# Kernel tuning notes

Hardware: AMD Instinct MI355X
Metric: run time of the kernel (lower is better)

The kernel has to match this reference:

```python
import jax, jax.numpy as jnp
import numpy as np

INPUT_SIZE = (224, 224)


def setup_inputs() -> dict:
    key = jax.random.key(0)
    k1, k2, k3 = jax.random.split(key, 3)
    feat2 = jax.random.normal(k1, (16, 512, 28, 28), dtype=jnp.float32)
    feat3 = jax.random.normal(k2, (16, 1024, 14, 14), dtype=jnp.float32)
    memory_bank = jax.random.normal(k3, (16384, 1536), dtype=jnp.float32)
    return {"feat2": feat2, "feat3": feat3, "memory_bank": memory_bank}


def reference(feat2, feat3, memory_bank):
    b, c2, h, w = feat2.shape
    c3 = feat3.shape[1]
    # interpolate(feat3, size=(h,w), mode='bilinear', align_corners=False)
    feat3_up = jax.image.resize(feat3, (b, c3, h, w), method='bilinear')
    features = jnp.concatenate([feat2, feat3_up], axis=1)  # [b, c, h, w]
    c = c2 + c3
    feats = features.transpose(0, 2, 3, 1).reshape(-1, c)  # [N, c]
    x_sq = jnp.sum(feats * feats, axis=1, keepdims=True)            # [N, 1]
    m_sq = jnp.sum(memory_bank * memory_bank, axis=1)[None, :]      # [1, M]
    d2 = x_sq + m_sq - 2.0 * (feats @ memory_bank.T)                # [N, M]
    min_d = jnp.sqrt(jnp.maximum(jnp.min(d2, axis=1), 0.0))         # [N]
    anomaly_map = min_d.reshape(b, 1, h, w)
    anomaly_map = jax.image.resize(
        anomaly_map, (b, 1, INPUT_SIZE[0], INPUT_SIZE[1]), method='bilinear')
    pred_score = jnp.max(anomaly_map.reshape(b, -1), axis=1)
    return anomaly_map, pred_score
```

## Files before the change

kernel.cpp:

```cpp
#include <hip/hip_runtime.h>
#include <math.h>

#define N_ROWS 12544
#define C_DIM  1536
#define M_ROWS 16384
#define BATCH  16

#define QS    16.0f
#define S2x2  0.0078125f
#define S2    0.00390625f

typedef int   i32x4 __attribute__((ext_vector_type(4)));
typedef unsigned char u8;
typedef signed char   i8;

__device__ __forceinline__ unsigned fkey(float f) {
  unsigned u = __float_as_uint(f);
  return (u & 0x80000000u) ? ~u : (u | 0x80000000u);
}
__device__ __forceinline__ float funkey(unsigned k) {
  unsigned u = (k & 0x80000000u) ? (k ^ 0x80000000u) : ~k;
  return __uint_as_float(u);
}

__device__ __forceinline__ void gl_lds16(const void* g, void* l) {
  __builtin_amdgcn_global_load_lds(
      (__attribute__((address_space(1))) void*)(g),
      (__attribute__((address_space(3))) void*)(l), 16, 0, 0);
}

__device__ __forceinline__ int quant(float v) {
  int q = __float2int_rn(v * QS);
  return max(-127, min(127, q));
}

__global__ void prep_all(const float* __restrict__ feat2,
                         const float* __restrict__ feat3,
                         const float* __restrict__ mb,
                         i8* __restrict__ feats, i8* __restrict__ mbb,
                         float* __restrict__ xsq, float* __restrict__ msq,
                         unsigned* __restrict__ dmin,
                         unsigned* __restrict__ score) {
  const int blk = blockIdx.x;
  const int t = threadIdx.x;
  __shared__ float sred[4];

  if (blk < M_ROWS) {
    const int j = blk;
    const float* in = mb + (size_t)j * C_DIM;
    i8* outp = mbb + (size_t)j * C_DIM;
    float ssq = 0.f;
    {
      const float4 v = *(const float4*)(in + t * 4);
      int q0 = quant(v.x), q1 = quant(v.y), q2 = quant(v.z), q3 = quant(v.w);
      unsigned w = (unsigned)(q0 & 0xFF) | ((unsigned)(q1 & 0xFF) << 8)
                 | ((unsigned)(q2 & 0xFF) << 16) | ((unsigned)(q3 & 0xFF) << 24);
      *(unsigned*)(outp + t * 4) = w;
      ssq = (float)(q0*q0 + q1*q1 + q2*q2 + q3*q3);
    }
    if (t < 128) {
      const int i2 = 256 + t;
      const float4 v = *(const float4*)(in + i2 * 4);
      int q0 = quant(v.x), q1 = quant(v.y), q2 = quant(v.z), q3 = quant(v.w);
      unsigned w = (unsigned)(q0 & 0xFF) | ((unsigned)(q1 & 0xFF) << 8)
                 | ((unsigned)(q2 & 0xFF) << 16) | ((unsigned)(q3 & 0xFF) << 24);
      *(unsigned*)(outp + i2 * 4) = w;
      ssq += (float)(q0*q0 + q1*q1 + q2*q2 + q3*q3);
    }
    for (int off = 32; off > 0; off >>= 1) ssq += __shfl_down(ssq, off, 64);
    if ((t & 63) == 0) sred[t >> 6] = ssq;
    __syncthreads();
    if (t == 0) msq[j] = S2 * (sred[0] + sred[1] + sred[2] + sred[3]);
  } else {
    const int n = blk - M_ROWS;
    const int b = n / 784;
    const int rem = n % 784;
    const int y = rem / 28, x = rem % 28;
    const float sy = 0.5f * y - 0.25f;
    const float sx = 0.5f * x - 0.25f;
    const int y0 = (int)floorf(sy); const float fy = sy - (float)y0;
    const int x0 = (int)floorf(sx); const float fx = sx - (float)x0;
    const int y0c = max(y0, 0), y1c = min(y0 + 1, 13);
    const int x0c = max(x0, 0), x1c = min(x0 + 1, 13);
    const float w00 = (1.f-fy)*(1.f-fx), w01 = (1.f-fy)*fx;
    const float w10 = fy*(1.f-fx),       w11 = fy*fx;

    float ssq = 0.f;
    i8* orow = feats + (size_t)n * C_DIM;
    for (int c = t; c < C_DIM; c += 256) {
      float v;
      if (c < 512) {
        v = feat2[(((size_t)b * 512 + c) * 28 + y) * 28 + x];
      } else {
        const float* f3 = feat3 + ((size_t)b * 1024 + (c - 512)) * 196;
        v = w00 * f3[y0c*14 + x0c] + w01 * f3[y0c*14 + x1c]
          + w10 * f3[y1c*14 + x0c] + w11 * f3[y1c*14 + x1c];
      }
      int q = quant(v);
      orow[c] = (i8)q;
      ssq += (float)(q * q);
    }
    for (int off = 32; off > 0; off >>= 1) ssq += __shfl_down(ssq, off, 64);
    if ((t & 63) == 0) sred[t >> 6] = ssq;
    __syncthreads();
    if (t == 0) {
      xsq[n] = S2 * (sred[0] + sred[1] + sred[2] + sred[3]);
      dmin[n] = 0xFFFFFFFFu;
    }
    if (n == 0 && t < BATCH) score[t] = 0u;
  }
}

__global__ void gemm_min(const i8* __restrict__ X, const i8* __restrict__ Mb,
                         const float* __restrict__ msq,
                         unsigned* __restrict__ dmin) {
  __shared__ u8 As[16384];
  __shared__ u8 Bs[16384];
  __shared__ unsigned smin[128];
  const int t = threadIdx.x;
  const int mtile = blockIdx.x;
  const int ntile = blockIdx.y;
  const int lane = t & 63, wave = t >> 6;
  const int wm = wave >> 1, wn = wave & 1;
  if (t < 128) smin[t] = 0xFFFFFFFFu;

  const int row0 = ntile * 128;
  const int col0 = mtile * 128;
  const int s_row = t >> 2;
  const int s_ch  = (t & 3) ^ ((t >> 3) & 3);
  const i8* ga = X  + (size_t)(row0 + s_row) * C_DIM + s_ch * 16;
  const i8* gb = Mb + (size_t)(col0 + s_row) * C_DIM + s_ch * 16;
  u8* la = As + t * 16;
  u8* lb = Bs + t * 16;

  i32x4 acc[4][4];
  const i32x4 zero = {0, 0, 0, 0};
#pragma unroll
  for (int mi = 0; mi < 4; mi++)
#pragma unroll
    for (int ni = 0; ni < 4; ni++) acc[mi][ni] = zero;

  const int quad = lane >> 4, l16 = lane & 15;
  const int fsw = (l16 >> 1) & 3;
  const int slot = ((quad ^ fsw) * 16);
  const u8* arow = As + (wm * 64 + l16) * 64 + slot;
  const u8* brow = Bs + (wn * 64 + l16) * 64 + slot;

  for (int k0 = 0; k0 < C_DIM; k0 += 128) {
    __syncthreads();
    gl_lds16(ga + k0,                    la);
    gl_lds16(ga + 64 * C_DIM + k0,       la + 4096);
    gl_lds16(ga + k0 + 64,               la + 8192);
    gl_lds16(ga + 64 * C_DIM + k0 + 64,  la + 12288);
    gl_lds16(gb + k0,                    lb);
    gl_lds16(gb + 64 * C_DIM + k0,       lb + 4096);
    gl_lds16(gb + k0 + 64,               lb + 8192);
    gl_lds16(gb + 64 * C_DIM + k0 + 64,  lb + 12288);
    __syncthreads();
#pragma unroll
    for (int sub = 0; sub < 2; sub++) {
      i32x4 af[4], bf[4];
#pragma unroll
      for (int mi = 0; mi < 4; mi++)
        af[mi] = *(const i32x4*)(arow + sub * 8192 + mi * 1024);
#pragma unroll
      for (int ni = 0; ni < 4; ni++)
        bf[ni] = *(const i32x4*)(brow + sub * 8192 + ni * 1024);
#pragma unroll
      for (int mi = 0; mi < 4; mi++)
#pragma unroll
        for (int ni = 0; ni < 4; ni++)
          acc[mi][ni] = __builtin_amdgcn_mfma_i32_16x16x64_i8(
              af[mi], bf[ni], acc[mi][ni], 0, 0, 0);
    }
  }

  float msql[4];
#pragma unroll
  for (int ni = 0; ni < 4; ni++)
    msql[ni] = msq[col0 + wn * 64 + ni * 16 + l16];

#pragma unroll
  for (int mi = 0; mi < 4; mi++) {
#pragma unroll
    for (int r = 0; r < 4; r++) {
      float v = msql[0] - S2x2 * (float)acc[mi][0][r];
#pragma unroll
      for (int ni = 1; ni < 4; ni++)
        v = fminf(v, msql[ni] - S2x2 * (float)acc[mi][ni][r]);
      v = fminf(v, __shfl_xor(v, 1, 64));
      v = fminf(v, __shfl_xor(v, 2, 64));
      v = fminf(v, __shfl_xor(v, 4, 64));
      v = fminf(v, __shfl_xor(v, 8, 64));
      if (l16 == 0) {
        int lrow = wm * 64 + mi * 16 + quad * 4 + r;
        atomicMin(&smin[lrow], fkey(v));
      }
    }
  }
  __syncthreads();
  if (t < 128) atomicMin(&dmin[row0 + t], smin[t]);
}

__global__ void finalize(const unsigned* __restrict__ dmin,
                         const float* __restrict__ xsq,
                         float* __restrict__ out) {
  const int b = blockIdx.x, slice = blockIdx.y, t = threadIdx.x;
  __shared__ float smap[784];
  __shared__ float sred[4];
  for (int i = t; i < 784; i += 256) {
    float d2 = xsq[b * 784 + i] + funkey(dmin[b * 784 + i]);
    smap[i] = sqrtf(fmaxf(d2, 0.f));
  }
  __syncthreads();
  float* omap = out + (size_t)b * 50176;
  float tmax = 0.f;
  const int p0 = slice * 6272;
  for (int p = p0 + t; p < p0 + 6272; p += 256) {
    const int Y = p / 224, Xp = p % 224;
    const float sy = Y * 0.125f - 0.4375f;
    const float sx = Xp * 0.125f - 0.4375f;
    const int y0 = (int)floorf(sy); const float fy = sy - (float)y0;
    const int x0 = (int)floorf(sx); const float fx = sx - (float)x0;
    const int y0c = max(y0, 0), y1c = min(y0 + 1, 27);
    const int x0c = max(x0, 0), x1c = min(x0 + 1, 27);
    float v = (1.f-fy)*((1.f-fx)*smap[y0c*28+x0c] + fx*smap[y0c*28+x1c])
            +      fy *((1.f-fx)*smap[y1c*28+x0c] + fx*smap[y1c*28+x1c]);
    omap[p] = v;
    tmax = fmaxf(tmax, v);
  }
  for (int off = 32; off > 0; off >>= 1)
    tmax = fmaxf(tmax, __shfl_down(tmax, off, 64));
  if ((t & 63) == 0) sred[t >> 6] = tmax;
  __syncthreads();
  if (t == 0) {
    float m = fmaxf(fmaxf(sred[0], sred[1]), fmaxf(sred[2], sred[3]));
    atomicMax((unsigned*)(out + 802816 + b), __float_as_uint(m));
  }
}

extern "C" void kernel_launch(void* const* d_in, const int* in_sizes, int n_in,
                              void* d_out, int out_size, void* d_ws, size_t ws_size,
                              hipStream_t stream) {
  const float* feat2 = (const float*)d_in[0];
  const float* feat3 = (const float*)d_in[1];
  const float* mb    = (const float*)d_in[2];
  char* ws = (char*)d_ws;
  i8*       feats = (i8*)ws;
  i8*       mbb   = (i8*)(ws + 19267584);
  float*    xsq   = (float*)(ws + 44433408);
  float*    msq   = (float*)(ws + 44483584);
  unsigned* dmin  = (unsigned*)(ws + 44549120);
  float* out = (float*)d_out;

  prep_all<<<M_ROWS + N_ROWS, 256, 0, stream>>>(
      feat2, feat3, mb, feats, mbb, xsq, msq, dmin,
      (unsigned*)(out + 802816));
  gemm_min<<<dim3(128, 98), 256, 0, stream>>>(feats, mbb, msq, dmin);
  finalize<<<dim3(BATCH, 8), 256, 0, stream>>>(dmin, xsq, out);
}
```

Before: 592.5 us.

## Restructure feature prep to process 28-pixel rows per block with packed writes

The feature-preparation path now assigns one block per (batch, image row) instead of one block per pixel. Each wave handles 7 pixels and each lane 4 consecutive channels, packs the quantized int8 values into 32-bit stores, and reduces the squared norm per pixel with wave shuffles instead of shared memory. The feature blocks are also moved ahead of the memory-bank blocks in the grid. The aim is to cut the strided per-pixel gathers, the byte-wide stores and the launch of 12544 tiny blocks. The trade-off is higher register use per thread and far fewer, heavier blocks.

Result: slower. 609.9 us (+2.9%).

```diff
diff --git a/kernel.cpp b/kernel.cpp
--- a/kernel.cpp
+++ b/kernel.cpp
@@ -5,6 +5,7 @@
 #define C_DIM  1536
 #define M_ROWS 16384
 #define BATCH  16
+#define FBLKS  448
 
 #define QS    16.0f
 #define S2x2  0.0078125f
@@ -43,12 +44,96 @@
                          unsigned* __restrict__ score) {
   const int blk = blockIdx.x;
   const int t = threadIdx.x;
-  __shared__ float sred[4];
-
-  if (blk < M_ROWS) {
-    const int j = blk;
+
+  if (blk < FBLKS) {
+    const int fb = blk;
+    const int b = fb / 28, y = fb % 28;
+    const int lane = t & 63, w = t >> 6;
+    const float sy = 0.5f * y - 0.25f;
+    const int y0 = (int)floorf(sy);
+    const float fy = sy - (float)y0;
+    const int y0c = max(y0, 0), y1c = min(y0 + 1, 13);
+
+    int pxl[7], x0l[7], x1l[7];
+    float wxa[7], wxb[7];
+#pragma unroll
+    for (int j = 0; j < 7; j++) {
+      const int px = w + 4 * j;
+      pxl[j] = px;
+      const float sx = 0.5f * px - 0.25f;
+      const int x0 = (int)floorf(sx);
+      const float fx = sx - (float)x0;
+      x0l[j] = max(x0, 0);
+      x1l[j] = min(x0 + 1, 13);
+      wxa[j] = 1.f - fx;
+      wxb[j] = fx;
+    }
+
+    float ssum[7];
+#pragma unroll
+    for (int j = 0; j < 7; j++) ssum[j] = 0.f;
+
+    const size_t n0 = (size_t)fb * 28;
+    for (int tile = 0; tile < 6; tile++) {
+      const int cbase = tile * 256 + 4 * lane;
+      unsigned pack[7];
+      if (tile < 2) {
+        const float* s0 = feat2 + (((size_t)b * 512 + cbase) * 28 + y) * 28;
+#pragma unroll
+        for (int j = 0; j < 7; j++) {
+          unsigned pk = 0;
+          float ss = 0.f;
+#pragma unroll
+          for (int k = 0; k < 4; k++) {
+            const float v = s0[k * 784 + pxl[j]];
+            const int q = quant(v);
+            pk |= ((unsigned)(q & 0xFF)) << (8 * k);
+            ss += (float)(q * q);
+          }
+          pack[j] = pk;
+          ssum[j] += ss;
+        }
+      } else {
+        const float* f3 = feat3 + ((size_t)b * 1024 + (cbase - 512)) * 196;
+#pragma unroll
+        for (int j = 0; j < 7; j++) {
+          unsigned pk = 0;
+          float ss = 0.f;
+#pragma unroll
+          for (int k = 0; k < 4; k++) {
+            const float* r0 = f3 + k * 196 + y0c * 14;
+            const float* r1 = f3 + k * 196 + y1c * 14;
+            const float h0 = wxa[j] * r0[x0l[j]] + wxb[j] * r0[x1l[j]];
+            const float h1 = wxa[j] * r1[x0l[j]] + wxb[j] * r1[x1l[j]];
+            const float v = (1.f - fy) * h0 + fy * h1;
+            const int q = quant(v);
+            pk |= ((unsigned)(q & 0xFF)) << (8 * k);
+            ss += (float)(q * q);
+          }
+          pack[j] = pk;
+          ssum[j] += ss;
+        }
+      }
+#pragma unroll
+      for (int j = 0; j < 7; j++)
+        *(unsigned*)(feats + (n0 + pxl[j]) * C_DIM + tile * 256 + 4 * lane) =
+            pack[j];
+    }
+#pragma unroll
+    for (int j = 0; j < 7; j++) {
+      float v = ssum[j];
+      for (int off = 32; off > 0; off >>= 1) v += __shfl_down(v, off, 64);
+      if (lane == 0) {
+        xsq[n0 + pxl[j]] = S2 * v;
+        dmin[n0 + pxl[j]] = 0xFFFFFFFFu;
+      }
+    }
+    if (blk == 0 && t < BATCH) score[t] = 0u;
+  } else {
+    const int j = blk - FBLKS;
     const float* in = mb + (size_t)j * C_DIM;
     i8* outp = mbb + (size_t)j * C_DIM;
+    __shared__ float sred[4];
     float ssq = 0.f;
     {
       const float4 v = *(const float4*)(in + t * 4);
@@ -71,43 +156,6 @@
     if ((t & 63) == 0) sred[t >> 6] = ssq;
     __syncthreads();
     if (t == 0) msq[j] = S2 * (sred[0] + sred[1] + sred[2] + sred[3]);
-  } else {
-    const int n = blk - M_ROWS;
-    const int b = n / 784;
-    const int rem = n % 784;
-    const int y = rem / 28, x = rem % 28;
-    const float sy = 0.5f * y - 0.25f;
-    const float sx = 0.5f * x - 0.25f;
-    const int y0 = (int)floorf(sy); const float fy = sy - (float)y0;
-    const int x0 = (int)floorf(sx); const float fx = sx - (float)x0;
-    const int y0c = max(y0, 0), y1c = min(y0 + 1, 13);
-    const int x0c = max(x0, 0), x1c = min(x0 + 1, 13);
-    const float w00 = (1.f-fy)*(1.f-fx), w01 = (1.f-fy)*fx;
-    const float w10 = fy*(1.f-fx),       w11 = fy*fx;
-
-    float ssq = 0.f;
-    i8* orow = feats + (size_t)n * C_DIM;
-    for (int c = t; c < C_DIM; c += 256) {
-      float v;
-      if (c < 512) {
-        v = feat2[(((size_t)b * 512 + c) * 28 + y) * 28 + x];
-      } else {
-        const float* f3 = feat3 + ((size_t)b * 1024 + (c - 512)) * 196;
-        v = w00 * f3[y0c*14 + x0c] + w01 * f3[y0c*14 + x1c]
-          + w10 * f3[y1c*14 + x0c] + w11 * f3[y1c*14 + x1c];
-      }
-      int q = quant(v);
-      orow[c] = (i8)q;
-      ssq += (float)(q * q);
-    }
-    for (int off = 32; off > 0; off >>= 1) ssq += __shfl_down(ssq, off, 64);
-    if ((t & 63) == 0) sred[t >> 6] = ssq;
-    __syncthreads();
-    if (t == 0) {
-      xsq[n] = S2 * (sred[0] + sred[1] + sred[2] + sred[3]);
-      dmin[n] = 0xFFFFFFFFu;
-    }
-    if (n == 0 && t < BATCH) score[t] = 0u;
   }
 }
 
@@ -253,7 +301,7 @@
   unsigned* dmin  = (unsigned*)(ws + 44549120);
   float* out = (float*)d_out;
 
-  prep_all<<<M_ROWS + N_ROWS, 256, 0, stream>>>(
+  prep_all<<<FBLKS + M_ROWS, 256, 0, stream>>>(
       feat2, feat3, mb, feats, mbb, xsq, msq, dmin,
       (unsigned*)(out + 802816));
   gemm_min<<<dim3(128, 98), 256, 0, stream>>>(feats, mbb, msq, dmin);
```
